# Kernel optimization log

Measured on AMD Instinct MI355X. Metric: run time of the kernel, lower is better.

Reference implementation:

```python
import jax, jax.numpy as jnp
import numpy as np

NUM_HEADS = 16
INPUT_SIZE = 1024
KEY_SIZE = 64
VALUE_SIZE = 64
LN_EPS = 1e-5


def setup_inputs() -> dict:
    key = jax.random.key(0)
    ks = jax.random.split(key, 11)
    B, S, D = 2, 2048, INPUT_SIZE
    Hk = NUM_HEADS * KEY_SIZE
    Hv = NUM_HEADS * VALUE_SIZE
    s = 0.02
    return {
        "queries": jax.random.normal(ks[0], (B, S, D), dtype=jnp.float32),
        "Wq": jax.random.normal(ks[1], (D, Hk), dtype=jnp.float32) * s,
        "bq": jnp.zeros((Hk,), dtype=jnp.float32),
        "Wk": jax.random.normal(ks[2], (D, Hk), dtype=jnp.float32) * s,
        "bk": jnp.zeros((Hk,), dtype=jnp.float32),
        "Wv": jax.random.normal(ks[3], (D, Hv), dtype=jnp.float32) * s,
        "bv": jnp.zeros((Hv,), dtype=jnp.float32),
        "Wo": jax.random.normal(ks[4], (Hv, D), dtype=jnp.float32) * s,
        "bo": jnp.zeros((D,), dtype=jnp.float32),
        "ln_gamma": jnp.ones((D,), dtype=jnp.float32),
        "ln_beta": jnp.zeros((D,), dtype=jnp.float32),
    }


def reference(queries, Wq, bq, Wk, bk, Wv, bv, Wo, bo, ln_gamma, ln_beta):
    B, S, D = queries.shape
    H, dk, dv = NUM_HEADS, KEY_SIZE, VALUE_SIZE
    residual = queries
    # projections -> [B, S, H, d]
    q = (queries @ Wq + bq).reshape(B, S, H, dk)
    k = (queries @ Wk + bk).reshape(B, S, H, dk)
    v = (queries @ Wv + bv).reshape(B, S, H, dv)
    # scaled dot-product attention per head
    scores = jnp.einsum("bqhd,bkhd->bhqk", q, k) / jnp.sqrt(jnp.float32(dk))
    attn = jax.nn.softmax(scores, axis=-1)
    out = jnp.einsum("bhqk,bkhd->bqhd", attn, v).reshape(B, S, H * dv)
    # out projection + residual + layernorm (dropout=0 / eval)
    res = out @ Wo + bo + residual
    mu = jnp.mean(res, axis=-1, keepdims=True)
    var = jnp.var(res, axis=-1, keepdims=True)
    return (res - mu) / jnp.sqrt(var + LN_EPS) * ln_gamma + ln_beta
```

## Files before the change

kernel.cpp:

```cpp
#include <hip/hip_runtime.h>
#include <hip/hip_bf16.h>
#include <math.h>

#define D 1024
#define NH 16
#define DK 64
#define LN_EPS 1e-5f
typedef __hip_bfloat16 bf16;
typedef __attribute__((ext_vector_type(8))) short bf16x8;
typedef __attribute__((ext_vector_type(4))) short short4v;
typedef __attribute__((ext_vector_type(4))) float f32x4;
typedef __attribute__((ext_vector_type(2))) unsigned int uint2v;

__device__ inline float tofloat(bf16 x) { return __bfloat162float(x); }
__device__ inline float tofs(short s) {
    bf16 b; __builtin_memcpy(&b, &s, 2);
    return __bfloat162float(b);
}
__device__ inline short bfbits(float v) {
    bf16 b = __float2bfloat16(v);
    short s; __builtin_memcpy(&s, &b, 2);
    return s;
}
__device__ inline unsigned int pk2(float a, float b) {
    float2 f2; f2.x = a; f2.y = b;
    __hip_bfloat162 h = __float22bfloat162_rn(f2);
    unsigned int u; __builtin_memcpy(&u, &h, 4);
    return u;
}
__device__ inline short4v pk4(float a, float b, float c, float d) {
    uint2v u; u[0] = pk2(a, b); u[1] = pk2(c, d);
    short4v s; __builtin_memcpy(&s, &u, 8);
    return s;
}

__device__ inline int wave_isf32(const unsigned short* __restrict__ Xu) {
    unsigned short u = Xu[threadIdx.x & 63];
    unsigned long long m = __ballot(((u >> 7) & 0xFF) >= 0x90);
    return __popcll(m) > 2;
}

template <typename T> __device__ inline T fromfloat(float v);
template <> __device__ inline float fromfloat<float>(float v) { return v; }
template <> __device__ inline bf16 fromfloat<bf16>(float v) { return __float2bfloat16(v); }

__global__ void prep_kernel(const void* X, const void* Wq, const void* Wk, const void* Wv,
                            const void* Wo, const void* bq, const void* bk, const void* bv,
                            const void* bo, const void* g, const void* be,
                            bf16* __restrict__ Xb, bf16* __restrict__ Wqkvt, bf16* __restrict__ Wot,
                            bf16* __restrict__ bqkv, bf16* __restrict__ bob,
                            bf16* __restrict__ gb, bf16* __restrict__ beb) {
    __shared__ float tile[64][65];
    const int isf32 = wave_isf32((const unsigned short*)X);
    const int bid = blockIdx.x;
    if (bid < 2048) {
        int e0 = bid * 2048 + threadIdx.x * 8;
        bf16x8 outv;
        if (isf32) {
            float4 v0 = ((const float4*)X)[e0 / 4];
            float4 v1 = ((const float4*)X)[e0 / 4 + 1];
            uint2v a, b;
            a[0] = pk2(v0.x, v0.y); a[1] = pk2(v0.z, v0.w);
            b[0] = pk2(v1.x, v1.y); b[1] = pk2(v1.z, v1.w);
            short4v s0, s1;
            __builtin_memcpy(&s0, &a, 8); __builtin_memcpy(&s1, &b, 8);
#pragma unroll
            for (int i = 0; i < 4; ++i) { outv[i] = s0[i]; outv[4 + i] = s1[i]; }
        } else {
            outv = ((const bf16x8*)X)[e0 / 8];
        }
        *(bf16x8*)(Xb + e0) = outv;
    } else if (bid < 3072) {
        int t = bid - 2048;
        int z = t >> 8, rem = t & 255;
        const void* srcs[4] = {Wq, Wk, Wv, Wo};
        const void* src = srcs[z];
        bf16* dst = (z < 3) ? (Wqkvt + (size_t)z * 1024 * 1024) : Wot;
        const int i0 = (rem >> 4) * 64, j0 = (rem & 15) * 64;
        const int r = threadIdx.x >> 2, c0 = (threadIdx.x & 3) * 16;
#pragma unroll
        for (int i = 0; i < 16; ++i) {
            int c = c0 + i;
            size_t idx = (size_t)(i0 + r) * 1024 + j0 + c;
            tile[r][c] = isf32 ? ((const float*)src)[idx] : tofloat(((const bf16*)src)[idx]);
        }
        __syncthreads();
#pragma unroll
        for (int i = 0; i < 16; ++i) {
            int c = c0 + i;
            dst[(size_t)(j0 + r) * 1024 + i0 + c] = __float2bfloat16(tile[c][r]);
        }
    } else {
        int idx = (bid - 3072) * 256 + threadIdx.x;
        int seg = idx >> 10, off = idx & 1023;
        const void* srcs[6] = {bq, bk, bv, bo, g, be};
        const void* src = srcs[seg];
        float v = isf32 ? ((const float*)src)[off] : tofloat(((const bf16*)src)[off]);
        bf16 bv16 = __float2bfloat16(v);
        if (seg < 3)       bqkv[seg * 1024 + off] = bv16;
        else if (seg == 3) bob[off] = bv16;
        else if (seg == 4) gb[off] = bv16;
        else               beb[off] = bv16;
    }
}

template <typename TC, bool RES, bool QS, bool VT>
__global__ __launch_bounds__(256) void mfma_gemm2(const bf16* __restrict__ A, const bf16* __restrict__ Bt,
                                                  const bf16* __restrict__ bias,
                                                  const bf16* __restrict__ residual,
                                                  TC* __restrict__ C, bf16* __restrict__ VtG,
                                                  int M, int N, int K, int S) {
    __shared__ short As[128][72];
    __shared__ short Bs[128][72];
    const int tid = threadIdx.x;
    const int lane = tid & 63, wave = tid >> 6;
    const int wy = wave >> 1, wx = wave & 1;
    const int mrow = lane & 15, quad = lane >> 4;
    const int bm = blockIdx.y * 128, bn = blockIdx.x * 128;

    f32x4 acc[4][4];
#pragma unroll
    for (int mi = 0; mi < 4; ++mi)
#pragma unroll
        for (int nt = 0; nt < 4; ++nt) acc[mi][nt] = (f32x4){0.f, 0.f, 0.f, 0.f};

    const int ra = tid >> 1, ca = (tid & 1) * 32;
    const bf16* aptr = A + (size_t)(bm + ra) * K + ca;
    const bf16* bptr = Bt + (size_t)(bn + ra) * K + ca;
    bf16x8 ar[4], br[4];
#pragma unroll
    for (int i = 0; i < 4; ++i) { ar[i] = *(const bf16x8*)(aptr + i * 8); br[i] = *(const bf16x8*)(bptr + i * 8); }

    for (int k0 = 0; k0 < K; k0 += 64) {
        __syncthreads();
#pragma unroll
        for (int i = 0; i < 4; ++i) {
            *(bf16x8*)&As[ra][ca + i * 8] = ar[i];
            *(bf16x8*)&Bs[ra][ca + i * 8] = br[i];
        }
        __syncthreads();
        if (k0 + 64 < K) {
#pragma unroll
            for (int i = 0; i < 4; ++i) {
                ar[i] = *(const bf16x8*)(aptr + k0 + 64 + i * 8);
                br[i] = *(const bf16x8*)(bptr + k0 + 64 + i * 8);
            }
        }
#pragma unroll
        for (int ks = 0; ks < 2; ++ks) {
            bf16x8 a[4], b[4];
#pragma unroll
            for (int mi = 0; mi < 4; ++mi)
                a[mi] = *(const bf16x8*)&As[wy * 64 + mi * 16 + mrow][ks * 32 + quad * 8];
#pragma unroll
            for (int nt = 0; nt < 4; ++nt)
                b[nt] = *(const bf16x8*)&Bs[wx * 64 + nt * 16 + mrow][ks * 32 + quad * 8];
#pragma unroll
            for (int mi = 0; mi < 4; ++mi)
#pragma unroll
                for (int nt = 0; nt < 4; ++nt)
                    acc[mi][nt] = __builtin_amdgcn_mfma_f32_16x16x32_bf16(a[mi], b[nt], acc[mi][nt], 0, 0, 0);
        }
    }
#pragma unroll
    for (int mi = 0; mi < 4; ++mi) {
#pragma unroll
        for (int nt = 0; nt < 4; ++nt) {
            int col = bn + wx * 64 + nt * 16 + mrow;
            float bc = tofloat(bias[col]);
            if (VT && col >= 2048) {
                int dvf = col - 2048, hh = dvf >> 6, dv = dvf & 63;
                int row0 = bm + wy * 64 + mi * 16 + quad * 4;
                int bb = row0 / S, key0 = row0 % S;
                short4v pk = pk4(acc[mi][nt][0] + bc, acc[mi][nt][1] + bc,
                                 acc[mi][nt][2] + bc, acc[mi][nt][3] + bc);
                *(short4v*)(VtG + (size_t)(bb * NH + hh) * S * 64 + (key0 >> 2) * 256 + dv * 4) = pk;
            } else {
                float sc = (QS && col < 1024) ? 0.18033688f : 1.0f;
#pragma unroll
                for (int reg = 0; reg < 4; ++reg) {
                    int row = bm + wy * 64 + mi * 16 + quad * 4 + reg;
                    float v = (acc[mi][nt][reg] + bc) * sc;
                    if (RES) v += tofloat(residual[(size_t)row * N + col]);
                    C[(size_t)row * N + col] = fromfloat<TC>(v);
                }
            }
        }
    }
}

__global__ __launch_bounds__(256) void attn_mfma(const bf16* __restrict__ QKV,
                                                 const bf16* __restrict__ VtG,
                                                 bf16* __restrict__ Op, float* __restrict__ Lp,
                                                 int S, int M) {
    __shared__ short Ks[64][72];
    __shared__ short Vs2[16 * 256];
    const int tid = threadIdx.x;
    const int lane = tid & 63, wave = tid >> 6;
    const int mrow = lane & 15, quad = lane >> 4;
    const int ldq = 3 * D;
    const int nqc = S / 128;
    const int bh = blockIdx.x / nqc, qc = blockIdx.x % nqc;
    const int b = bh / NH, h = bh % NH;
    const int q0 = qc * 128 + wave * 32;
    const int sp = blockIdx.y;
    const int Sh = S / 2, kvlo = sp * Sh;

    bf16x8 qf[2][2];
#pragma unroll
    for (int qt = 0; qt < 2; ++qt) {
        const bf16* qbase = QKV + ((size_t)(b * S + q0 + qt * 16 + mrow)) * ldq + h * DK;
        qf[qt][0] = *(const bf16x8*)(qbase + quad * 8);
        qf[qt][1] = *(const bf16x8*)(qbase + 32 + quad * 8);
    }

    f32x4 o[2][4];
#pragma unroll
    for (int qt = 0; qt < 2; ++qt)
#pragma unroll
        for (int t = 0; t < 4; ++t) o[qt][t] = (f32x4){0.f, 0.f, 0.f, 0.f};
    float lsum[2] = {0.f, 0.f};

    const int rs_ = tid >> 2, cs_ = (tid & 3) * 16;
    const bf16* kb0 = QKV + ((size_t)(b * S + kvlo + rs_)) * ldq + D + h * DK + cs_;
    const bf16* vb0 = VtG + (size_t)(b * NH + h) * S * 64 + kvlo * 64 + tid * 16;
    const int kg_l = tid >> 4, dv0 = (tid & 15) * 4;
    const int voff = kg_l * 256 + (((dv0 + kg_l * 8) & 63) * 4);
    bf16x8 kr0 = *(const bf16x8*)kb0, kr1 = *(const bf16x8*)(kb0 + 8);
    bf16x8 vr0 = *(const bf16x8*)vb0, vr1 = *(const bf16x8*)(vb0 + 8);

    for (int kc = 0; kc < Sh; kc += 64) {
        __syncthreads();
        *(bf16x8*)&Ks[rs_][cs_] = kr0;
        *(bf16x8*)&Ks[rs_][cs_ + 8] = kr1;
        *(bf16x8*)&Vs2[voff] = vr0;
        *(bf16x8*)&Vs2[voff + 8] = vr1;
        __syncthreads();
        if (kc + 64 < Sh) {
            const bf16* kn = kb0 + (size_t)(kc + 64) * ldq;
            kr0 = *(const bf16x8*)kn; kr1 = *(const bf16x8*)(kn + 8);
            const bf16* vn = vb0 + (size_t)(kc + 64) * 64;
            vr0 = *(const bf16x8*)vn; vr1 = *(const bf16x8*)(vn + 8);
        }

        f32x4 s[2][4];
#pragma unroll
        for (int qt = 0; qt < 2; ++qt)
#pragma unroll
            for (int t = 0; t < 4; ++t) s[qt][t] = (f32x4){0.f, 0.f, 0.f, 0.f};
#pragma unroll
        for (int ks = 0; ks < 2; ++ks) {
#pragma unroll
            for (int t = 0; t < 4; ++t) {
                bf16x8 kf = *(const bf16x8*)&Ks[t * 16 + mrow][ks * 32 + quad * 8];
                s[0][t] = __builtin_amdgcn_mfma_f32_16x16x32_bf16(kf, qf[0][ks], s[0][t], 0, 0, 0);
                s[1][t] = __builtin_amdgcn_mfma_f32_16x16x32_bf16(kf, qf[1][ks], s[1][t], 0, 0, 0);
            }
        }
        short4v pf[2][4];
#pragma unroll
        for (int qt = 0; qt < 2; ++qt)
#pragma unroll
            for (int t = 0; t < 4; ++t) {
                float p0 = __builtin_amdgcn_exp2f(s[qt][t][0]);
                float p1 = __builtin_amdgcn_exp2f(s[qt][t][1]);
                float p2 = __builtin_amdgcn_exp2f(s[qt][t][2]);
                float p3 = __builtin_amdgcn_exp2f(s[qt][t][3]);
                lsum[qt] += (p0 + p1) + (p2 + p3);
                pf[qt][t] = pk4(p0, p1, p2, p3);
            }
#pragma unroll
        for (int kt = 0; kt < 4; ++kt) {
            const int kg = kt * 4 + quad;
#pragma unroll
            for (int dvt = 0; dvt < 4; ++dvt) {
                int dvs = ((dvt * 16 + mrow) + kg * 8) & 63;
                short4v vf = *(const short4v*)&Vs2[kg * 256 + dvs * 4];
                o[0][dvt] = __builtin_amdgcn_mfma_f32_16x16x16bf16_1k(pf[0][kt], vf, o[0][dvt], 0, 0, 0);
                o[1][dvt] = __builtin_amdgcn_mfma_f32_16x16x16bf16_1k(pf[1][kt], vf, o[1][dvt], 0, 0, 0);
            }
        }
    }
#pragma unroll
    for (int qt = 0; qt < 2; ++qt) {
        float v = lsum[qt];
        v += __shfl_xor(v, 16, 64);
        v += __shfl_xor(v, 32, 64);
        lsum[qt] = v;
        if (quad == 0) Lp[(size_t)sp * M + b * S + q0 + qt * 16 + mrow] = v;
    }
#pragma unroll
    for (int qt = 0; qt < 2; ++qt)
#pragma unroll
        for (int r = 0; r < 4; ++r) {
            bf16* orow = Op + (size_t)sp * M * D +
                         ((size_t)(b * S + q0 + qt * 16 + quad * 4 + r)) * D + h * DK;
#pragma unroll
            for (int dvt = 0; dvt < 4; ++dvt)
                orow[dvt * 16 + mrow] = __float2bfloat16(o[qt][dvt][r]);
        }
}

__global__ void combine_kernel(const bf16* __restrict__ Op, const float* __restrict__ Lp,
                               bf16* __restrict__ Ob, int M) {
    int idx = blockIdx.x * 256 + threadIdx.x;
    int row = idx >> 7;
    size_t e0 = (size_t)row * D + (idx & 127) * 8;
    bf16x8 o0 = *(const bf16x8*)(Op + e0);
    bf16x8 o1 = *(const bf16x8*)(Op + (size_t)M * D + e0);
    float inv = 1.0f / (Lp[row] + Lp[M + row]);
    float f[8];
#pragma unroll
    for (int i = 0; i < 8; ++i) f[i] = (tofs(o0[i]) + tofs(o1[i])) * inv;
    bf16x8 outv;
    short4v a = pk4(f[0], f[1], f[2], f[3]), b2 = pk4(f[4], f[5], f[6], f[7]);
#pragma unroll
    for (int i = 0; i < 4; ++i) { outv[i] = a[i]; outv[4 + i] = b2[i]; }
    *(bf16x8*)(Ob + e0) = outv;
}

__global__ void ln_kernel(const float* __restrict__ R, const bf16* __restrict__ gamma,
                          const bf16* __restrict__ beta, void* __restrict__ out,
                          const void* __restrict__ X) {
    __shared__ float red[8];
    const int isf32 = wave_isf32((const unsigned short*)X);
    const int row = blockIdx.x;
    const float4 xv = *(const float4*)(R + (size_t)row * D + threadIdx.x * 4);
    float sum = xv.x + xv.y + xv.z + xv.w;
    float sq = xv.x * xv.x + xv.y * xv.y + xv.z * xv.z + xv.w * xv.w;
    for (int off = 32; off; off >>= 1) {
        sum += __shfl_xor(sum, off, 64);
        sq += __shfl_xor(sq, off, 64);
    }
    const int wave = threadIdx.x / 64, lane = threadIdx.x % 64;
    if (lane == 0) { red[wave] = sum; red[wave + 4] = sq; }
    __syncthreads();
    sum = red[0] + red[1] + red[2] + red[3];
    sq = red[4] + red[5] + red[6] + red[7];
    const float mu = sum / (float)D;
    const float var = sq / (float)D - mu * mu;
    const float inv = rsqrtf(var + LN_EPS);
    const float x4[4] = {xv.x, xv.y, xv.z, xv.w};
#pragma unroll
    for (int i = 0; i < 4; ++i) {
        int cidx = threadIdx.x * 4 + i;
        float y = (x4[i] - mu) * inv * tofloat(gamma[cidx]) + tofloat(beta[cidx]);
        size_t oidx = (size_t)row * D + cidx;
        if (isf32) ((float*)out)[oidx] = y;
        else       ((bf16*)out)[oidx] = __float2bfloat16(y);
    }
}

extern "C" void kernel_launch(void* const* d_in, const int* in_sizes, int n_in,
                              void* d_out, int out_size, void* d_ws, size_t ws_size,
                              hipStream_t stream) {
    const int M = in_sizes[0] / D;
    const int B = 2;
    const int S = M / B;

    char* p = (char*)d_ws;
    auto alloc = [&](size_t bytes) { char* r = p; p += (bytes + 255) & ~(size_t)255; return r; };
    bf16* Xb    = (bf16*)alloc((size_t)M * D * 2);
    bf16* Wqkvt = (bf16*)alloc((size_t)3 * D * D * 2);
    bf16* Wot   = (bf16*)alloc((size_t)D * D * 2);
    bf16* bqkv  = (bf16*)alloc(3 * D * 2);
    bf16* bob   = (bf16*)alloc(D * 2);
    bf16* gb    = (bf16*)alloc(D * 2);
    bf16* beb   = (bf16*)alloc(D * 2);
    bf16* QKV   = (bf16*)alloc((size_t)M * 3 * D * 2);
    bf16* VtG   = (bf16*)alloc((size_t)M * D * 2);
    bf16* Opart = (bf16*)alloc((size_t)2 * M * D * 2);
    float* Lp   = (float*)alloc((size_t)2 * M * 4);
    bf16* Ob    = (bf16*)alloc((size_t)M * D * 2);
    float* Rf   = (float*)alloc((size_t)M * D * 4);

    prep_kernel<<<3096, 256, 0, stream>>>(d_in[0], d_in[1], d_in[3], d_in[5], d_in[7],
                                          d_in[2], d_in[4], d_in[6], d_in[8], d_in[9], d_in[10],
                                          Xb, Wqkvt, Wot, bqkv, bob, gb, beb);

    mfma_gemm2<bf16, false, true, true><<<dim3(3 * D / 128, M / 128), 256, 0, stream>>>(
        Xb, Wqkvt, bqkv, nullptr, QKV, VtG, M, 3 * D, D, S);

    attn_mfma<<<dim3(B * NH * (S / 128), 2), 256, 0, stream>>>(QKV, VtG, Opart, Lp, S, M);

    combine_kernel<<<M * D / 8 / 256, 256, 0, stream>>>(Opart, Lp, Ob, M);

    mfma_gemm2<float, true, false, false><<<dim3(D / 128, M / 128), 256, 0, stream>>>(
        Ob, Wot, bob, Xb, Rf, nullptr, M, D, D, S);

    ln_kernel<<<M, 256, 0, stream>>>(Rf, gb, beb, d_out, d_in[0]);
}
```

Before: 234.7 us.

## Load A and K fragments directly from global into registers, retile out-projection

The QKV and output GEMMs now load A-operand MFMA fragments straight from global memory into double-buffered registers instead of staging them in LDS. The output GEMM also uses a 128x64 tile so more blocks are launched. The attention kernel does the same for K fragments and double-buffers V in LDS, which removes one barrier per iteration. The prep kernel vectorizes its weight transpose loads and stores. These changes cut LDS traffic and barriers, at the cost of more register pressure and less coalesced global reads for A and K.

Result: slower. 589.2 us (+151.1%).

```diff
diff --git a/kernel.cpp b/kernel.cpp
--- a/kernel.cpp
+++ b/kernel.cpp
@@ -17,11 +17,6 @@
     bf16 b; __builtin_memcpy(&b, &s, 2);
     return __bfloat162float(b);
 }
-__device__ inline short bfbits(float v) {
-    bf16 b = __float2bfloat16(v);
-    short s; __builtin_memcpy(&s, &b, 2);
-    return s;
-}
 __device__ inline unsigned int pk2(float a, float b) {
     float2 f2; f2.x = a; f2.y = b;
     __hip_bfloat162 h = __float22bfloat162_rn(f2);
@@ -32,6 +27,17 @@
     uint2v u; u[0] = pk2(a, b); u[1] = pk2(c, d);
     short4v s; __builtin_memcpy(&s, &u, 8);
     return s;
+}
+__device__ inline bf16x8 pk8(const float* f) {
+    uint2v a, b;
+    a[0] = pk2(f[0], f[1]); a[1] = pk2(f[2], f[3]);
+    b[0] = pk2(f[4], f[5]); b[1] = pk2(f[6], f[7]);
+    bf16x8 o;
+    short4v s0, s1;
+    __builtin_memcpy(&s0, &a, 8); __builtin_memcpy(&s1, &b, 8);
+#pragma unroll
+    for (int i = 0; i < 4; ++i) { o[i] = s0[i]; o[4 + i] = s1[i]; }
+    return o;
 }
 
 __device__ inline int wave_isf32(const unsigned short* __restrict__ Xu) {
@@ -53,19 +59,15 @@
     __shared__ float tile[64][65];
     const int isf32 = wave_isf32((const unsigned short*)X);
     const int bid = blockIdx.x;
+    const int tid = threadIdx.x;
     if (bid < 2048) {
-        int e0 = bid * 2048 + threadIdx.x * 8;
+        int e0 = bid * 2048 + tid * 8;
         bf16x8 outv;
         if (isf32) {
             float4 v0 = ((const float4*)X)[e0 / 4];
             float4 v1 = ((const float4*)X)[e0 / 4 + 1];
-            uint2v a, b;
-            a[0] = pk2(v0.x, v0.y); a[1] = pk2(v0.z, v0.w);
-            b[0] = pk2(v1.x, v1.y); b[1] = pk2(v1.z, v1.w);
-            short4v s0, s1;
-            __builtin_memcpy(&s0, &a, 8); __builtin_memcpy(&s1, &b, 8);
-#pragma unroll
-            for (int i = 0; i < 4; ++i) { outv[i] = s0[i]; outv[4 + i] = s1[i]; }
+            float f[8] = {v0.x, v0.y, v0.z, v0.w, v1.x, v1.y, v1.z, v1.w};
+            outv = pk8(f);
         } else {
             outv = ((const bf16x8*)X)[e0 / 8];
         }
@@ -77,21 +79,32 @@
         const void* src = srcs[z];
         bf16* dst = (z < 3) ? (Wqkvt + (size_t)z * 1024 * 1024) : Wot;
         const int i0 = (rem >> 4) * 64, j0 = (rem & 15) * 64;
-        const int r = threadIdx.x >> 2, c0 = (threadIdx.x & 3) * 16;
-#pragma unroll
-        for (int i = 0; i < 16; ++i) {
-            int c = c0 + i;
-            size_t idx = (size_t)(i0 + r) * 1024 + j0 + c;
-            tile[r][c] = isf32 ? ((const float*)src)[idx] : tofloat(((const bf16*)src)[idx]);
-        }
-        __syncthreads();
-#pragma unroll
-        for (int i = 0; i < 16; ++i) {
-            int c = c0 + i;
-            dst[(size_t)(j0 + r) * 1024 + i0 + c] = __float2bfloat16(tile[c][r]);
+        const int tr = tid >> 4, tc4 = (tid & 15) * 4;
+#pragma unroll
+        for (int p = 0; p < 4; ++p) {
+            int r = p * 16 + tr;
+            if (isf32) {
+                float4 v = *(const float4*)((const float*)src + (size_t)(i0 + r) * 1024 + j0 + tc4);
+                tile[r][tc4] = v.x; tile[r][tc4 + 1] = v.y;
+                tile[r][tc4 + 2] = v.z; tile[r][tc4 + 3] = v.w;
+            } else {
+                short4v v = *(const short4v*)((const bf16*)src + (size_t)(i0 + r) * 1024 + j0 + tc4);
+#pragma unroll
+                for (int q = 0; q < 4; ++q) tile[r][tc4 + q] = tofs(v[q]);
+            }
+        }
+        __syncthreads();
+        const int wj = tid >> 3, wi = (tid & 7) * 8;
+#pragma unroll
+        for (int p = 0; p < 2; ++p) {
+            int j = p * 32 + wj;
+            float f[8];
+#pragma unroll
+            for (int q = 0; q < 8; ++q) f[q] = tile[wi + q][j];
+            *(bf16x8*)(dst + (size_t)(j0 + j) * 1024 + i0 + wi) = pk8(f);
         }
     } else {
-        int idx = (bid - 3072) * 256 + threadIdx.x;
+        int idx = (bid - 3072) * 256 + tid;
         int seg = idx >> 10, off = idx & 1023;
         const void* srcs[6] = {bq, bk, bv, bo, g, be};
         const void* src = srcs[seg];
@@ -104,13 +117,10 @@
     }
 }
 
-template <typename TC, bool RES, bool QS, bool VT>
-__global__ __launch_bounds__(256) void mfma_gemm2(const bf16* __restrict__ A, const bf16* __restrict__ Bt,
-                                                  const bf16* __restrict__ bias,
-                                                  const bf16* __restrict__ residual,
-                                                  TC* __restrict__ C, bf16* __restrict__ VtG,
-                                                  int M, int N, int K, int S) {
-    __shared__ short As[128][72];
+__global__ __launch_bounds__(256) void gemm_qkv(const bf16* __restrict__ A, const bf16* __restrict__ Bt,
+                                                const bf16* __restrict__ bias,
+                                                bf16* __restrict__ C, bf16* __restrict__ VtG,
+                                                int M, int N, int K, int S) {
     __shared__ short Bs[128][72];
     const int tid = threadIdx.x;
     const int lane = tid & 63, wave = tid >> 6;
@@ -124,34 +134,40 @@
 #pragma unroll
         for (int nt = 0; nt < 4; ++nt) acc[mi][nt] = (f32x4){0.f, 0.f, 0.f, 0.f};
 
-    const int ra = tid >> 1, ca = (tid & 1) * 32;
-    const bf16* aptr = A + (size_t)(bm + ra) * K + ca;
-    const bf16* bptr = Bt + (size_t)(bn + ra) * K + ca;
-    bf16x8 ar[4], br[4];
-#pragma unroll
-    for (int i = 0; i < 4; ++i) { ar[i] = *(const bf16x8*)(aptr + i * 8); br[i] = *(const bf16x8*)(bptr + i * 8); }
-
+    const int rb = tid >> 1, cb = (tid & 1) * 32;
+    const bf16* bptr = Bt + (size_t)(bn + rb) * K + cb;
+    bf16x8 br[4];
+#pragma unroll
+    for (int i = 0; i < 4; ++i) br[i] = *(const bf16x8*)(bptr + i * 8);
+
+    const bf16* aptr[4];
+#pragma unroll
+    for (int mi = 0; mi < 4; ++mi)
+        aptr[mi] = A + (size_t)(bm + wy * 64 + mi * 16 + mrow) * K + quad * 8;
+    bf16x8 af[2][2][4];
+#pragma unroll
+    for (int ks = 0; ks < 2; ++ks)
+#pragma unroll
+        for (int mi = 0; mi < 4; ++mi) af[0][ks][mi] = *(const bf16x8*)(aptr[mi] + ks * 32);
+
+    int par = 0;
     for (int k0 = 0; k0 < K; k0 += 64) {
         __syncthreads();
 #pragma unroll
-        for (int i = 0; i < 4; ++i) {
-            *(bf16x8*)&As[ra][ca + i * 8] = ar[i];
-            *(bf16x8*)&Bs[ra][ca + i * 8] = br[i];
-        }
+        for (int i = 0; i < 4; ++i) *(bf16x8*)&Bs[rb][cb + i * 8] = br[i];
         __syncthreads();
         if (k0 + 64 < K) {
 #pragma unroll
-            for (int i = 0; i < 4; ++i) {
-                ar[i] = *(const bf16x8*)(aptr + k0 + 64 + i * 8);
-                br[i] = *(const bf16x8*)(bptr + k0 + 64 + i * 8);
-            }
+            for (int i = 0; i < 4; ++i) br[i] = *(const bf16x8*)(bptr + k0 + 64 + i * 8);
+#pragma unroll
+            for (int ks = 0; ks < 2; ++ks)
+#pragma unroll
+                for (int mi = 0; mi < 4; ++mi)
+                    af[par ^ 1][ks][mi] = *(const bf16x8*)(aptr[mi] + k0 + 64 + ks * 32);
         }
 #pragma unroll
         for (int ks = 0; ks < 2; ++ks) {
-            bf16x8 a[4], b[4];
-#pragma unroll
-            for (int mi = 0; mi < 4; ++mi)
-                a[mi] = *(const bf16x8*)&As[wy * 64 + mi * 16 + mrow][ks * 32 + quad * 8];
+            bf16x8 b[4];
 #pragma unroll
             for (int nt = 0; nt < 4; ++nt)
                 b[nt] = *(const bf16x8*)&Bs[wx * 64 + nt * 16 + mrow][ks * 32 + quad * 8];
@@ -159,8 +175,9 @@
             for (int mi = 0; mi < 4; ++mi)
 #pragma unroll
                 for (int nt = 0; nt < 4; ++nt)
-                    acc[mi][nt] = __builtin_amdgcn_mfma_f32_16x16x32_bf16(a[mi], b[nt], acc[mi][nt], 0, 0, 0);
-        }
+                    acc[mi][nt] = __builtin_amdgcn_mfma_f32_16x16x32_bf16(af[par][ks][mi], b[nt], acc[mi][nt], 0, 0, 0);
+        }
+        par ^= 1;
     }
 #pragma unroll
     for (int mi = 0; mi < 4; ++mi) {
@@ -168,7 +185,7 @@
         for (int nt = 0; nt < 4; ++nt) {
             int col = bn + wx * 64 + nt * 16 + mrow;
             float bc = tofloat(bias[col]);
-            if (VT && col >= 2048) {
+            if (col >= 2048) {
                 int dvf = col - 2048, hh = dvf >> 6, dv = dvf & 63;
                 int row0 = bm + wy * 64 + mi * 16 + quad * 4;
                 int bb = row0 / S, key0 = row0 % S;
@@ -176,14 +193,89 @@
                                  acc[mi][nt][2] + bc, acc[mi][nt][3] + bc);
                 *(short4v*)(VtG + (size_t)(bb * NH + hh) * S * 64 + (key0 >> 2) * 256 + dv * 4) = pk;
             } else {
-                float sc = (QS && col < 1024) ? 0.18033688f : 1.0f;
+                float sc = (col < 1024) ? 0.18033688f : 1.0f;
 #pragma unroll
                 for (int reg = 0; reg < 4; ++reg) {
                     int row = bm + wy * 64 + mi * 16 + quad * 4 + reg;
-                    float v = (acc[mi][nt][reg] + bc) * sc;
-                    if (RES) v += tofloat(residual[(size_t)row * N + col]);
-                    C[(size_t)row * N + col] = fromfloat<TC>(v);
+                    C[(size_t)row * N + col] = __float2bfloat16((acc[mi][nt][reg] + bc) * sc);
                 }
+            }
+        }
+    }
+}
+
+__global__ __launch_bounds__(256) void gemm_out(const bf16* __restrict__ A, const bf16* __restrict__ Bt,
+                                                const bf16* __restrict__ bias,
+                                                const bf16* __restrict__ residual,
+                                                float* __restrict__ C, int M, int N, int K) {
+    __shared__ short Bs[64][72];
+    const int tid = threadIdx.x;
+    const int lane = tid & 63, wave = tid >> 6;
+    const int wy = wave >> 1, wx = wave & 1;
+    const int mrow = lane & 15, quad = lane >> 4;
+    const int bm = blockIdx.y * 128, bn = blockIdx.x * 64;
+
+    f32x4 acc[4][2];
+#pragma unroll
+    for (int mi = 0; mi < 4; ++mi)
+#pragma unroll
+        for (int nt = 0; nt < 2; ++nt) acc[mi][nt] = (f32x4){0.f, 0.f, 0.f, 0.f};
+
+    const int rb = tid >> 2, cb = (tid & 3) * 16;
+    const bf16* bptr = Bt + (size_t)(bn + rb) * K + cb;
+    bf16x8 br[2];
+#pragma unroll
+    for (int i = 0; i < 2; ++i) br[i] = *(const bf16x8*)(bptr + i * 8);
+
+    const bf16* aptr[4];
+#pragma unroll
+    for (int mi = 0; mi < 4; ++mi)
+        aptr[mi] = A + (size_t)(bm + wy * 64 + mi * 16 + mrow) * K + quad * 8;
+    bf16x8 af[2][2][4];
+#pragma unroll
+    for (int ks = 0; ks < 2; ++ks)
+#pragma unroll
+        for (int mi = 0; mi < 4; ++mi) af[0][ks][mi] = *(const bf16x8*)(aptr[mi] + ks * 32);
+
+    int par = 0;
+    for (int k0 = 0; k0 < K; k0 += 64) {
+        __syncthreads();
+#pragma unroll
+        for (int i = 0; i < 2; ++i) *(bf16x8*)&Bs[rb][cb + i * 8] = br[i];
+        __syncthreads();
+        if (k0 + 64 < K) {
+#pragma unroll
+            for (int i = 0; i < 2; ++i) br[i] = *(const bf16x8*)(bptr + k0 + 64 + i * 8);
+#pragma unroll
+            for (int ks = 0; ks < 2; ++ks)
+#pragma unroll
+                for (int mi = 0; mi < 4; ++mi)
+                    af[par ^ 1][ks][mi] = *(const bf16x8*)(aptr[mi] + k0 + 64 + ks * 32);
+        }
+#pragma unroll
+        for (int ks = 0; ks < 2; ++ks) {
+            bf16x8 b[2];
+#pragma unroll
+            for (int nt = 0; nt < 2; ++nt)
+                b[nt] = *(const bf16x8*)&Bs[wx * 32 + nt * 16 + mrow][ks * 32 + quad * 8];
+#pragma unroll
+            for (int mi = 0; mi < 4; ++mi)
+#pragma unroll
+                for (int nt = 0; nt < 2; ++nt)
+                    acc[mi][nt] = __builtin_amdgcn_mfma_f32_16x16x32_bf16(af[par][ks][mi], b[nt], acc[mi][nt], 0, 0, 0);
+        }
+        par ^= 1;
+    }
+#pragma unroll
+    for (int mi = 0; mi < 4; ++mi) {
+#pragma unroll
+        for (int nt = 0; nt < 2; ++nt) {
+            int col = bn + wx * 32 + nt * 16 + mrow;
+            float bc = tofloat(bias[col]);
+#pragma unroll
+            for (int reg = 0; reg < 4; ++reg) {
+                int row = bm + wy * 64 + mi * 16 + quad * 4 + reg;
+                C[(size_t)row * N + col] = acc[mi][nt][reg] + bc + tofloat(residual[(size_t)row * N + col]);
             }
         }
     }
@@ -193,8 +285,7 @@
                                                  const bf16* __restrict__ VtG,
                                                  bf16* __restrict__ Op, float* __restrict__ Lp,
                                                  int S, int M) {
-    __shared__ short Ks[64][72];
-    __shared__ short Vs2[16 * 256];
+    __shared__ short Vs2[2][16 * 256];
     const int tid = threadIdx.x;
     const int lane = tid & 63, wave = tid >> 6;
     const int mrow = lane & 15, quad = lane >> 4;
@@ -221,26 +312,33 @@
         for (int t = 0; t < 4; ++t) o[qt][t] = (f32x4){0.f, 0.f, 0.f, 0.f};
     float lsum[2] = {0.f, 0.f};
 
-    const int rs_ = tid >> 2, cs_ = (tid & 3) * 16;
-    const bf16* kb0 = QKV + ((size_t)(b * S + kvlo + rs_)) * ldq + D + h * DK + cs_;
+    const bf16* kfb = QKV + ((size_t)(b * S + kvlo + mrow)) * ldq + D + h * DK + quad * 8;
     const bf16* vb0 = VtG + (size_t)(b * NH + h) * S * 64 + kvlo * 64 + tid * 16;
     const int kg_l = tid >> 4, dv0 = (tid & 15) * 4;
     const int voff = kg_l * 256 + (((dv0 + kg_l * 8) & 63) * 4);
-    bf16x8 kr0 = *(const bf16x8*)kb0, kr1 = *(const bf16x8*)(kb0 + 8);
+
+    bf16x8 kf2[2][2][4];
+#pragma unroll
+    for (int ks = 0; ks < 2; ++ks)
+#pragma unroll
+        for (int t = 0; t < 4; ++t)
+            kf2[0][ks][t] = *(const bf16x8*)(kfb + (size_t)(t * 16) * ldq + ks * 32);
     bf16x8 vr0 = *(const bf16x8*)vb0, vr1 = *(const bf16x8*)(vb0 + 8);
 
-    for (int kc = 0; kc < Sh; kc += 64) {
-        __syncthreads();
-        *(bf16x8*)&Ks[rs_][cs_] = kr0;
-        *(bf16x8*)&Ks[rs_][cs_ + 8] = kr1;
-        *(bf16x8*)&Vs2[voff] = vr0;
-        *(bf16x8*)&Vs2[voff + 8] = vr1;
+    int par = 0;
+    for (int kc = 0; kc < Sh; kc += 64, par ^= 1) {
+        *(bf16x8*)&Vs2[par][voff] = vr0;
+        *(bf16x8*)&Vs2[par][voff + 8] = vr1;
         __syncthreads();
         if (kc + 64 < Sh) {
-            const bf16* kn = kb0 + (size_t)(kc + 64) * ldq;
-            kr0 = *(const bf16x8*)kn; kr1 = *(const bf16x8*)(kn + 8);
             const bf16* vn = vb0 + (size_t)(kc + 64) * 64;
             vr0 = *(const bf16x8*)vn; vr1 = *(const bf16x8*)(vn + 8);
+            const bf16* kn = kfb + (size_t)(kc + 64) * ldq;
+#pragma unroll
+            for (int ks = 0; ks < 2; ++ks)
+#pragma unroll
+                for (int t = 0; t < 4; ++t)
+                    kf2[par ^ 1][ks][t] = *(const bf16x8*)(kn + (size_t)(t * 16) * ldq + ks * 32);
         }
 
         f32x4 s[2][4];
@@ -252,9 +350,8 @@
         for (int ks = 0; ks < 2; ++ks) {
 #pragma unroll
             for (int t = 0; t < 4; ++t) {
-                bf16x8 kf = *(const bf16x8*)&Ks[t * 16 + mrow][ks * 32 + quad * 8];
-                s[0][t] = __builtin_amdgcn_mfma_f32_16x16x32_bf16(kf, qf[0][ks], s[0][t], 0, 0, 0);
-                s[1][t] = __builtin_amdgcn_mfma_f32_16x16x32_bf16(kf, qf[1][ks], s[1][t], 0, 0, 0);
+                s[0][t] = __builtin_amdgcn_mfma_f32_16x16x32_bf16(kf2[par][ks][t], qf[0][ks], s[0][t], 0, 0, 0);
+                s[1][t] = __builtin_amdgcn_mfma_f32_16x16x32_bf16(kf2[par][ks][t], qf[1][ks], s[1][t], 0, 0, 0);
             }
         }
         short4v pf[2][4];
@@ -275,7 +372,7 @@
 #pragma unroll
             for (int dvt = 0; dvt < 4; ++dvt) {
                 int dvs = ((dvt * 16 + mrow) + kg * 8) & 63;
-                short4v vf = *(const short4v*)&Vs2[kg * 256 + dvs * 4];
+                short4v vf = *(const short4v*)&Vs2[par][kg * 256 + dvs * 4];
                 o[0][dvt] = __builtin_amdgcn_mfma_f32_16x16x16bf16_1k(pf[0][kt], vf, o[0][dvt], 0, 0, 0);
                 o[1][dvt] = __builtin_amdgcn_mfma_f32_16x16x16bf16_1k(pf[1][kt], vf, o[1][dvt], 0, 0, 0);
             }
@@ -312,11 +409,7 @@
     float f[8];
 #pragma unroll
     for (int i = 0; i < 8; ++i) f[i] = (tofs(o0[i]) + tofs(o1[i])) * inv;
-    bf16x8 outv;
-    short4v a = pk4(f[0], f[1], f[2], f[3]), b2 = pk4(f[4], f[5], f[6], f[7]);
-#pragma unroll
-    for (int i = 0; i < 4; ++i) { outv[i] = a[i]; outv[4 + i] = b2[i]; }
-    *(bf16x8*)(Ob + e0) = outv;
+    *(bf16x8*)(Ob + e0) = pk8(f);
 }
 
 __global__ void ln_kernel(const float* __restrict__ R, const bf16* __restrict__ gamma,
@@ -378,15 +471,14 @@
                                           d_in[2], d_in[4], d_in[6], d_in[8], d_in[9], d_in[10],
                                           Xb, Wqkvt, Wot, bqkv, bob, gb, beb);
 
-    mfma_gemm2<bf16, false, true, true><<<dim3(3 * D / 128, M / 128), 256, 0, stream>>>(
-        Xb, Wqkvt, bqkv, nullptr, QKV, VtG, M, 3 * D, D, S);
+    gemm_qkv<<<dim3(3 * D / 128, M / 128), 256, 0, stream>>>(
+        Xb, Wqkvt, bqkv, QKV, VtG, M, 3 * D, D, S);
 
     attn_mfma<<<dim3(B * NH * (S / 128), 2), 256, 0, stream>>>(QKV, VtG, Opart, Lp, S, M);
 
     combine_kernel<<<M * D / 8 / 256, 256, 0, stream>>>(Opart, Lp, Ob, M);
 
-    mfma_gemm2<float, true, false, false><<<dim3(D / 128, M / 128), 256, 0, stream>>>(
-        Ob, Wot, bob, Xb, Rf, nullptr, M, D, D, S);
+    gemm_out<<<dim3(D / 64, M / 128), 256, 0, stream>>>(Ob, Wot, bob, Xb, Rf, M, D, D);
 
     ln_kernel<<<M, 256, 0, stream>>>(Rf, gb, beb, d_out, d_in[0]);
 }
```
